# Kernel optimization log

Hardware: AMD Instinct MI355X
Metric: run time of the kernel (lower is better)

The kernel has to match this reference:

```python
import jax, jax.numpy as jnp
import numpy as np

EPS = 1e-16

def setup_inputs() -> dict:
    key = jax.random.key(0)
    k1, k2, k3, k4, k5, k6 = jax.random.split(key, 6)
    B, S, NT, E = 8, 256, 50, 64
    # sorted event times in [0, 90); horizon T = 100 > all events; all valid (>=0)
    event_times = jnp.sort(jax.random.uniform(k1, (B, S), dtype=jnp.float32) * 90.0, axis=1)
    event_types = jax.random.randint(k2, (B, S), 0, NT)
    # parameters initialized N(0, 0.1) as in _initialize_parameters
    type_embeddings = 0.1 * jax.random.normal(k3, (NT, E), dtype=jnp.float32)
    a = 0.1 * jax.random.normal(k4, (NT, E), dtype=jnp.float32)
    A = 0.1 * jax.random.normal(k5, (NT, NT, E), dtype=jnp.float32)
    P = 0.1 * jax.random.normal(k6, (NT, NT, E), dtype=jnp.float32)
    return {"event_times": event_times, "event_types": event_types, "T": 100,
            "type_embeddings": type_embeddings, "a": a, "A": A, "P": P}

def _hawkes_nll(event_times, event_types, T, emb, a, A, P):
    B, S = event_times.shape
    NT, E = emb.shape
    Tf = jnp.asarray(T, jnp.float32)
    emb_t = emb[event_types]            # (B,S,E) embedding of each event's type
    a_t = a[event_types]                # (B,S,E)
    valid = event_times >= 0.0          # (B,S)

    # ---- log-likelihood: intensity of the observed type at each event time ----
    # pairwise: axis 1 = query event i, axis 2 = history event j (j < i)
    dt = event_times[:, :, None] - event_times[:, None, :]                 # (B,Si,Sj)
    hist_mask = (jnp.arange(S)[:, None] > jnp.arange(S)[None, :])[None]    # (1,Si,Sj): j<i
    # A_pair[b,i,j,e] = A[type_j, type_i, e]; same for P_pair
    A_pair = A[event_types[:, None, :], event_types[:, :, None]]           # (B,Si,Sj,E)
    P_pair = P[event_types[:, None, :], event_types[:, :, None]]
    emb_i = emb_t[:, :, None, :]                                           # (B,Si,1,E)
    emb_j = emb_t[:, None, :, :]                                           # (B,1,Sj,E)
    decay = jnp.exp(-(emb_i * P_pair) * emb_j * dt[..., None])
    contrib = (emb_i * A_pair) * decay * emb_j                             # (B,Si,Sj,E)
    m = jnp.sum(jnp.where(hist_mask[..., None], contrib, 0.0), axis=2)     # (B,Si,E)
    inten = jnp.sum(jax.nn.softplus(emb_t * a_t + m), axis=-1)             # (B,S)
    ll = jnp.sum(jnp.where(valid, jnp.log(inten + EPS), 0.0))

    # ---- integral approximation (as in compute_loss) ----
    # intensity at horizon T for ALL types, using full valid history
    dT = Tf - event_times                                                  # (B,S)
    A_all = A[event_types]                                                 # (B,S,NT,E): A[t_j, t, e]
    P_all = P[event_types]
    decT = jnp.exp(-(emb[None, None] * P_all) * emb_t[:, :, None, :] * dT[:, :, None, None])
    conT = (emb[None, None] * A_all) * decT * emb_t[:, :, None, :]         # (B,S,NT,E)
    m_T = jnp.sum(jnp.where(valid[:, :, None, None], conT, 0.0), axis=1)   # (B,NT,E)
    inten_T = jnp.sum(jax.nn.softplus(emb * a + m_T), axis=(-2, -1))       # (B,)

    base_sum = jnp.sum(jax.nn.softplus(emb * a))                           # empty-history intensity summed over types
    any_valid = jnp.any(valid, axis=1)                                     # (B,)
    last_time = jnp.where(any_valid, jnp.max(jnp.where(valid, event_times, -1e30), axis=1), 0.0)
    first_time = jnp.where(any_valid, jnp.min(jnp.where(valid, event_times, 1e30), axis=1), 0.0)
    integ_b = jnp.where(any_valid,
                        inten_T * (Tf - last_time) + base_sum * first_time,
                        base_sum * Tf)
    integral = jnp.sum(integ_b)
    return -(ll - integral)

def reference(event_times, event_types, T, type_embeddings, a, A, P):
    return _hawkes_nll(event_times, event_types, T, type_embeddings, a, A, P)
```

## Files before the change

### kernel.cpp

```cpp
#include <hip/hip_runtime.h>
#include <math.h>

#define B   8
#define S   256
#define NT  50
#define E   64
#define NTE (NT * E)
#define EPSF 1e-16f

#define NW        4
#define LL_BLOCKS (B * S / 2)
#define IN_BLOCKS (B * NT)

__device__ __forceinline__ float softplus(float x) {
    if (x > 20.0f) return x;
    return log1pf(__expf(x));
}

__device__ __forceinline__ float wave_reduce_sum(float v) {
    #pragma unroll
    for (int off = 32; off > 0; off >>= 1)
        v += __shfl_down(v, off, 64);
    return v;
}

__global__ __launch_bounds__(64 * NW) void main_kernel(
    const float* __restrict__ times, const int* __restrict__ types,
    const int* __restrict__ Tp,
    const float* __restrict__ emb,  const float* __restrict__ a,
    const float* __restrict__ Amat, const float* __restrict__ Pmat,
    float* __restrict__ ws_ll, float* __restrict__ ws_int)
{
    const int tid = threadIdx.x;
    const int e   = tid & 63;
    const int w   = tid >> 6;
    const int bid = blockIdx.x;
    const bool is_ll = (bid < LL_BLOCKS);
    const int b = is_ll ? (bid / (S / 2)) : ((bid - LL_BLOCKS) / NT);

    __shared__ __align__(16) float s_emb[NTE];
    __shared__ float2 s_ev[S];
    __shared__ float  s_part[2][NW][E];
    __shared__ float  s_row[2];

    {
        const float4* __restrict__ emb4 = (const float4*)emb;
        float4* s4 = (float4*)s_emb;
        for (int idx = tid; idx < NTE / 4; idx += 64 * NW)
            s4[idx] = emb4[idx];
    }
    for (int j = tid; j < S; j += 64 * NW)
        s_ev[j] = make_float2(times[b * S + j], __int_as_float(types[b * S + j]));
    __syncthreads();

    if (is_ll) {
        const int ih = bid % (S / 2);
        const int rows[2] = { ih, S - 1 - ih };
        #pragma unroll
        for (int r = 0; r < 2; ++r) {
            const int   i     = rows[r];
            const float t_i   = s_ev[i].x;
            const int   ty_i  = __float_as_int(s_ev[i].y);
            const int   col   = ty_i * E + e;
            const float negEi = -s_emb[col];

            float macc = 0.0f;
            #pragma unroll 8
            for (int j = w; j < i; j += NW) {
                const float2 ev  = s_ev[j];
                const int   tyj  = __float_as_int(ev.y);
                const float dtj  = t_i - ev.x;
                const int   base = tyj * NTE + col;
                const float ej   = s_emb[tyj * E + e];
                const float Pe   = Pmat[base];
                const float Ae   = Amat[base];
                macc = fmaf(Ae * ej, __expf(negEi * Pe * ej * dtj), macc);
            }
            s_part[r][w][e] = macc;
        }
        __syncthreads();
        if (w < 2) {
            const int   i     = rows[w];
            const float t_i   = s_ev[i].x;
            const int   ty_i  = __float_as_int(s_ev[i].y);
            const int   col   = ty_i * E + e;
            const float emb_i = s_emb[col];
            float mt = 0.0f;
            #pragma unroll
            for (int q = 0; q < NW; ++q) mt += s_part[w][q][e];
            const float sp    = softplus(fmaf(emb_i, mt, emb_i * a[col]));
            const float inten = wave_reduce_sum(sp);
            if (e == 0)
                s_row[w] = (t_i >= 0.0f) ? logf(inten + EPSF) : 0.0f;
        }
        __syncthreads();
        if (tid == 0) ws_ll[bid] = s_row[0] + s_row[1];
    } else {
        const int   k    = (bid - LL_BLOCKS) % NT;
        const float Tf   = (float)(*Tp);
        const int   colk = k * E + e;
        const float embk = s_emb[colk];
        const float negEk = -embk;

        float acc = 0.0f;
        #pragma unroll 8
        for (int i = w; i < S; i += NW) {
            const float2 ev  = s_ev[i];
            const int   ty   = __float_as_int(ev.y);
            const float dT   = Tf - ev.x;
            const int   base = ty * NTE + colk;
            const float et   = s_emb[ty * E + e];
            const float c    = Amat[base] * et * __expf(negEk * Pmat[base] * et * dT);
            acc += (ev.x >= 0.0f) ? c : 0.0f;
        }
        s_part[0][w][e] = acc;
        __syncthreads();
        if (w == 0) {
            float mt = 0.0f;
            #pragma unroll
            for (int q = 0; q < NW; ++q) mt += s_part[0][q][e];
            const float sp = softplus(fmaf(embk, mt, embk * a[colk]));
            const float s  = wave_reduce_sum(sp);
            if (e == 0) ws_int[bid - LL_BLOCKS] = s;
        }
    }
}

__global__ __launch_bounds__(256) void finalize_kernel(
    const float* __restrict__ times,
    const int* __restrict__ Tp,
    const float* __restrict__ emb, const float* __restrict__ a,
    const float* __restrict__ ws_ll, const float* __restrict__ ws_int,
    float* __restrict__ out)
{
    const int t    = threadIdx.x;
    const int lane = t & 63;
    const int w    = t >> 6;
    const float Tf = (float)(*Tp);

    float llp = 0.0f;
    for (int idx = t; idx < LL_BLOCKS; idx += 256) llp += ws_ll[idx];
    float bs = 0.0f;
    for (int idx = t; idx < NTE; idx += 256) bs += softplus(emb[idx] * a[idx]);

    __shared__ float red[256], red2[256];
    red[t] = llp; red2[t] = bs;

    __shared__ float s_first[B], s_last[B], s_iT[B], s_any[B];
    for (int b = w; b < B; b += 4) {
        float mn = 1e30f, mx = -1e30f;
        #pragma unroll
        for (int q = 0; q < S / 64; ++q) {
            const float tv = times[b * S + q * 64 + lane];
            const bool valid = (tv >= 0.0f);
            mn = fminf(mn, valid ? tv : 1e30f);
            mx = fmaxf(mx, valid ? tv : -1e30f);
        }
        float iv = (lane < NT) ? ws_int[b * NT + lane] : 0.0f;
        #pragma unroll
        for (int off = 32; off > 0; off >>= 1) {
            mn = fminf(mn, __shfl_down(mn, off, 64));
            mx = fmaxf(mx, __shfl_down(mx, off, 64));
            iv += __shfl_down(iv, off, 64);
        }
        if (lane == 0) {
            const bool any_valid = (mn < 1e29f);
            s_any[b]   = any_valid ? 1.0f : 0.0f;
            s_first[b] = any_valid ? mn : 0.0f;
            s_last[b]  = any_valid ? mx : 0.0f;
            s_iT[b]    = iv;
        }
    }
    __syncthreads();

    for (int off = 128; off > 0; off >>= 1) {
        if (t < off) { red[t] += red[t + off]; red2[t] += red2[t + off]; }
        __syncthreads();
    }

    if (t == 0) {
        const float base_sum = red2[0];
        float integral = 0.0f;
        #pragma unroll
        for (int b = 0; b < B; ++b) {
            integral += (s_any[b] > 0.5f)
                ? s_iT[b] * (Tf - s_last[b]) + base_sum * s_first[b]
                : base_sum * Tf;
        }
        out[0] = integral - red[0];
    }
}

extern "C" void kernel_launch(void* const* d_in, const int* in_sizes, int n_in,
                              void* d_out, int out_size, void* d_ws, size_t ws_size,
                              hipStream_t stream) {
    const float* times = (const float*)d_in[0];
    const int*   types = (const int*)d_in[1];
    const int*   Tp    = (const int*)d_in[2];
    const float* emb   = (const float*)d_in[3];
    const float* a     = (const float*)d_in[4];
    const float* Amat  = (const float*)d_in[5];
    const float* Pmat  = (const float*)d_in[6];

    float* ws     = (float*)d_ws;
    float* ws_ll  = ws;
    float* ws_int = ws + LL_BLOCKS;
    float* out    = (float*)d_out;

    main_kernel<<<LL_BLOCKS + IN_BLOCKS, 64 * NW, 0, stream>>>(
        times, types, Tp, emb, a, Amat, Pmat, ws_ll, ws_int);
    finalize_kernel<<<1, 256, 0, stream>>>(times, Tp, emb, a, ws_ll, ws_int, out);
}
```

Baseline: 87.78 us.

## Fuse finalize into main kernel via last-block atomic and precompute type offsets

Removes the separate finalize kernel launch. Each block now increments a global counter, and the last block to finish runs the final reduction, then resets the counter. Event records in shared memory now hold precomputed type*E and type*NTE offsets so the inner loops skip the integer multiplies. The exponentials switch to exp2f with LOG2E folded into the per-row constant. The cost is one atomic and a threadfence per block, a wider shared-memory record, and reliance on the global counter being reset correctly between calls.

New measurement: 110.7 us. 26.1% more time.

```diff
diff --git a/kernel.cpp b/kernel.cpp
--- a/kernel.cpp
+++ b/kernel.cpp
@@ -7,10 +7,14 @@
 #define E   64
 #define NTE (NT * E)
 #define EPSF 1e-16f
+#define LOG2E 1.4426950408889634f
 
 #define NW        4
 #define LL_BLOCKS (B * S / 2)
 #define IN_BLOCKS (B * NT)
+#define NBLK      (LL_BLOCKS + IN_BLOCKS)
+
+__device__ int g_done = 0;
 
 __device__ __forceinline__ float softplus(float x) {
     if (x > 20.0f) return x;
@@ -29,7 +33,8 @@
     const int* __restrict__ Tp,
     const float* __restrict__ emb,  const float* __restrict__ a,
     const float* __restrict__ Amat, const float* __restrict__ Pmat,
-    float* __restrict__ ws_ll, float* __restrict__ ws_int)
+    float* __restrict__ ws_ll, float* __restrict__ ws_int,
+    float* __restrict__ out)
 {
     const int tid = threadIdx.x;
     const int e   = tid & 63;
@@ -38,10 +43,11 @@
     const bool is_ll = (bid < LL_BLOCKS);
     const int b = is_ll ? (bid / (S / 2)) : ((bid - LL_BLOCKS) / NT);
 
-    __shared__ __align__(16) float s_emb[NTE];
-    __shared__ float2 s_ev[S];
+    __shared__ __align__(16) float  s_emb[NTE];
+    __shared__ __align__(16) float4 s_ev[S];
     __shared__ float  s_part[2][NW][E];
     __shared__ float  s_row[2];
+    __shared__ int    s_fin;
 
     {
         const float4* __restrict__ emb4 = (const float4*)emb;
@@ -49,8 +55,12 @@
         for (int idx = tid; idx < NTE / 4; idx += 64 * NW)
             s4[idx] = emb4[idx];
     }
-    for (int j = tid; j < S; j += 64 * NW)
-        s_ev[j] = make_float2(times[b * S + j], __int_as_float(types[b * S + j]));
+    for (int j = tid; j < S; j += 64 * NW) {
+        const int ty = types[b * S + j];
+        s_ev[j] = make_float4(times[b * S + j],
+                              __int_as_float(ty * E),
+                              __int_as_float(ty * NTE), 0.0f);
+    }
     __syncthreads();
 
     if (is_ll) {
@@ -58,23 +68,21 @@
         const int rows[2] = { ih, S - 1 - ih };
         #pragma unroll
         for (int r = 0; r < 2; ++r) {
-            const int   i     = rows[r];
-            const float t_i   = s_ev[i].x;
-            const int   ty_i  = __float_as_int(s_ev[i].y);
-            const int   col   = ty_i * E + e;
-            const float negEi = -s_emb[col];
+            const int   i      = rows[r];
+            const float t_i    = s_ev[i].x;
+            const int   col    = __float_as_int(s_ev[i].y) + e;
+            const float negEi2 = -s_emb[col] * LOG2E;
 
             float macc = 0.0f;
             #pragma unroll 8
             for (int j = w; j < i; j += NW) {
-                const float2 ev  = s_ev[j];
-                const int   tyj  = __float_as_int(ev.y);
+                const float4 ev  = s_ev[j];
                 const float dtj  = t_i - ev.x;
-                const int   base = tyj * NTE + col;
-                const float ej   = s_emb[tyj * E + e];
+                const int   base = __float_as_int(ev.z) + col;
+                const float ej   = s_emb[__float_as_int(ev.y) + e];
                 const float Pe   = Pmat[base];
                 const float Ae   = Amat[base];
-                macc = fmaf(Ae * ej, __expf(negEi * Pe * ej * dtj), macc);
+                macc = fmaf(Ae * ej, exp2f(negEi2 * Pe * ej * dtj), macc);
             }
             s_part[r][w][e] = macc;
         }
@@ -82,8 +90,7 @@
         if (w < 2) {
             const int   i     = rows[w];
             const float t_i   = s_ev[i].x;
-            const int   ty_i  = __float_as_int(s_ev[i].y);
-            const int   col   = ty_i * E + e;
+            const int   col   = __float_as_int(s_ev[i].y) + e;
             const float emb_i = s_emb[col];
             float mt = 0.0f;
             #pragma unroll
@@ -96,21 +103,20 @@
         __syncthreads();
         if (tid == 0) ws_ll[bid] = s_row[0] + s_row[1];
     } else {
-        const int   k    = (bid - LL_BLOCKS) % NT;
-        const float Tf   = (float)(*Tp);
-        const int   colk = k * E + e;
-        const float embk = s_emb[colk];
-        const float negEk = -embk;
+        const int   k      = (bid - LL_BLOCKS) % NT;
+        const float Tf     = (float)(*Tp);
+        const int   colk   = k * E + e;
+        const float embk   = s_emb[colk];
+        const float negEk2 = -embk * LOG2E;
 
         float acc = 0.0f;
         #pragma unroll 8
         for (int i = w; i < S; i += NW) {
-            const float2 ev  = s_ev[i];
-            const int   ty   = __float_as_int(ev.y);
+            const float4 ev  = s_ev[i];
             const float dT   = Tf - ev.x;
-            const int   base = ty * NTE + colk;
-            const float et   = s_emb[ty * E + e];
-            const float c    = Amat[base] * et * __expf(negEk * Pmat[base] * et * dT);
+            const int   base = __float_as_int(ev.z) + colk;
+            const float et   = s_emb[__float_as_int(ev.y) + e];
+            const float c    = Amat[base] * et * exp2f(negEk2 * Pmat[base] * et * dT);
             acc += (ev.x >= 0.0f) ? c : 0.0f;
         }
         s_part[0][w][e] = acc;
@@ -124,39 +130,39 @@
             if (e == 0) ws_int[bid - LL_BLOCKS] = s;
         }
     }
-}
-
-__global__ __launch_bounds__(256) void finalize_kernel(
-    const float* __restrict__ times,
-    const int* __restrict__ Tp,
-    const float* __restrict__ emb, const float* __restrict__ a,
-    const float* __restrict__ ws_ll, const float* __restrict__ ws_int,
-    float* __restrict__ out)
-{
-    const int t    = threadIdx.x;
-    const int lane = t & 63;
-    const int w    = t >> 6;
+
+    if (tid == 0) {
+        __threadfence();
+        const int old = atomicAdd(&g_done, 1);
+        s_fin = (old == NBLK - 1) ? 1 : 0;
+    }
+    __syncthreads();
+    if (s_fin == 0) return;
+
+    __threadfence();
+
     const float Tf = (float)(*Tp);
 
     float llp = 0.0f;
-    for (int idx = t; idx < LL_BLOCKS; idx += 256) llp += ws_ll[idx];
+    for (int idx = tid; idx < LL_BLOCKS; idx += 256) llp += ws_ll[idx];
     float bs = 0.0f;
-    for (int idx = t; idx < NTE; idx += 256) bs += softplus(emb[idx] * a[idx]);
+    for (int idx = tid; idx < NTE; idx += 256) bs += softplus(s_emb[idx] * a[idx]);
 
     __shared__ float red[256], red2[256];
-    red[t] = llp; red2[t] = bs;
-
-    __shared__ float s_first[B], s_last[B], s_iT[B], s_any[B];
-    for (int b = w; b < B; b += 4) {
+    red[tid] = llp; red2[tid] = bs;
+
+    __shared__ float s_first[B], s_lastt[B], s_iT[B], s_any[B];
+    const int lane = tid & 63;
+    for (int bb = w; bb < B; bb += NW) {
         float mn = 1e30f, mx = -1e30f;
         #pragma unroll
         for (int q = 0; q < S / 64; ++q) {
-            const float tv = times[b * S + q * 64 + lane];
+            const float tv = times[bb * S + q * 64 + lane];
             const bool valid = (tv >= 0.0f);
             mn = fminf(mn, valid ? tv : 1e30f);
             mx = fmaxf(mx, valid ? tv : -1e30f);
         }
-        float iv = (lane < NT) ? ws_int[b * NT + lane] : 0.0f;
+        float iv = (lane < NT) ? ws_int[bb * NT + lane] : 0.0f;
         #pragma unroll
         for (int off = 32; off > 0; off >>= 1) {
             mn = fminf(mn, __shfl_down(mn, off, 64));
@@ -165,29 +171,30 @@
         }
         if (lane == 0) {
             const bool any_valid = (mn < 1e29f);
-            s_any[b]   = any_valid ? 1.0f : 0.0f;
-            s_first[b] = any_valid ? mn : 0.0f;
-            s_last[b]  = any_valid ? mx : 0.0f;
-            s_iT[b]    = iv;
+            s_any[bb]   = any_valid ? 1.0f : 0.0f;
+            s_first[bb] = any_valid ? mn : 0.0f;
+            s_lastt[bb] = any_valid ? mx : 0.0f;
+            s_iT[bb]    = iv;
         }
     }
     __syncthreads();
 
     for (int off = 128; off > 0; off >>= 1) {
-        if (t < off) { red[t] += red[t + off]; red2[t] += red2[t + off]; }
-        __syncthreads();
-    }
-
-    if (t == 0) {
+        if (tid < off) { red[tid] += red[tid + off]; red2[tid] += red2[tid + off]; }
+        __syncthreads();
+    }
+
+    if (tid == 0) {
         const float base_sum = red2[0];
         float integral = 0.0f;
         #pragma unroll
-        for (int b = 0; b < B; ++b) {
-            integral += (s_any[b] > 0.5f)
-                ? s_iT[b] * (Tf - s_last[b]) + base_sum * s_first[b]
+        for (int bb = 0; bb < B; ++bb) {
+            integral += (s_any[bb] > 0.5f)
+                ? s_iT[bb] * (Tf - s_lastt[bb]) + base_sum * s_first[bb]
                 : base_sum * Tf;
         }
         out[0] = integral - red[0];
+        atomicExch(&g_done, 0);
     }
 }
 
@@ -207,7 +214,6 @@
     float* ws_int = ws + LL_BLOCKS;
     float* out    = (float*)d_out;
 
-    main_kernel<<<LL_BLOCKS + IN_BLOCKS, 64 * NW, 0, stream>>>(
-        times, types, Tp, emb, a, Amat, Pmat, ws_ll, ws_int);
-    finalize_kernel<<<1, 256, 0, stream>>>(times, Tp, emb, a, ws_ll, ws_int, out);
-}
+    main_kernel<<<NBLK, 64 * NW, 0, stream>>>(
+        times, types, Tp, emb, a, Amat, Pmat, ws_ll, ws_int, out);
+}
```

## Stage per-row A/P slices in shared memory and use 8 waves per block

Applied to the files above, without the earlier changes.

Each block preloads the A and P columns for its query types (all source types) into LDS as interleaved float2. The inner loops then read from LDS instead of gathering from global memory. The block size doubles to 8 waves, and the exponential becomes exp2f with log2e folded into the scale. This adds large per-block staging traffic and about 51KB of LDS, which limits occupancy and may exceed the work the loop itself does.

Result: slower. 98.00 us (+11.6%).

```diff
diff --git a/kernel.cpp b/kernel.cpp
--- a/kernel.cpp
+++ b/kernel.cpp
@@ -7,8 +7,10 @@
 #define E   64
 #define NTE (NT * E)
 #define EPSF 1e-16f
-
-#define NW        4
+#define LOG2E 1.4426950408889634f
+
+#define NW        8
+#define NTHREADS  (64 * NW)
 #define LL_BLOCKS (B * S / 2)
 #define IN_BLOCKS (B * NT)
 
@@ -24,7 +26,7 @@
     return v;
 }
 
-__global__ __launch_bounds__(64 * NW) void main_kernel(
+__global__ __launch_bounds__(NTHREADS) void main_kernel(
     const float* __restrict__ times, const int* __restrict__ types,
     const int* __restrict__ Tp,
     const float* __restrict__ emb,  const float* __restrict__ a,
@@ -38,19 +40,40 @@
     const bool is_ll = (bid < LL_BLOCKS);
     const int b = is_ll ? (bid / (S / 2)) : ((bid - LL_BLOCKS) / NT);
 
-    __shared__ __align__(16) float s_emb[NTE];
+    __shared__ __align__(16) float  s_emb[NTE];
+    __shared__ __align__(16) float2 s_AP[2][NTE];
     __shared__ float2 s_ev[S];
     __shared__ float  s_part[2][NW][E];
     __shared__ float  s_row[2];
 
+    int ty0, ty1;
+    if (is_ll) {
+        const int ih = bid % (S / 2);
+        ty0 = types[b * S + ih];
+        ty1 = types[b * S + (S - 1 - ih)];
+    } else {
+        ty0 = (bid - LL_BLOCKS) % NT;
+        ty1 = ty0;
+    }
+
     {
         const float4* __restrict__ emb4 = (const float4*)emb;
         float4* s4 = (float4*)s_emb;
-        for (int idx = tid; idx < NTE / 4; idx += 64 * NW)
+        for (int idx = tid; idx < NTE / 4; idx += NTHREADS)
             s4[idx] = emb4[idx];
     }
-    for (int j = tid; j < S; j += 64 * NW)
-        s_ev[j] = make_float2(times[b * S + j], __int_as_float(types[b * S + j]));
+    for (int idx = tid; idx < NTE; idx += NTHREADS) {
+        const int row = idx >> 6, col = idx & 63;
+        const int g0 = row * NTE + ty0 * E + col;
+        s_AP[0][idx] = make_float2(Amat[g0], Pmat[g0]);
+        if (is_ll) {
+            const int g1 = row * NTE + ty1 * E + col;
+            s_AP[1][idx] = make_float2(Amat[g1], Pmat[g1]);
+        }
+    }
+    for (int j = tid; j < S; j += NTHREADS)
+        s_ev[j] = make_float2(times[b * S + j],
+                              __int_as_float(types[b * S + j] * E));
     __syncthreads();
 
     if (is_ll) {
@@ -58,23 +81,20 @@
         const int rows[2] = { ih, S - 1 - ih };
         #pragma unroll
         for (int r = 0; r < 2; ++r) {
-            const int   i     = rows[r];
-            const float t_i   = s_ev[i].x;
-            const int   ty_i  = __float_as_int(s_ev[i].y);
-            const int   col   = ty_i * E + e;
-            const float negEi = -s_emb[col];
+            const int   i      = rows[r];
+            const float t_i    = s_ev[i].x;
+            const int   col    = __float_as_int(s_ev[i].y) + e;
+            const float negEi2 = -s_emb[col] * LOG2E;
 
             float macc = 0.0f;
             #pragma unroll 8
             for (int j = w; j < i; j += NW) {
-                const float2 ev  = s_ev[j];
-                const int   tyj  = __float_as_int(ev.y);
-                const float dtj  = t_i - ev.x;
-                const int   base = tyj * NTE + col;
-                const float ej   = s_emb[tyj * E + e];
-                const float Pe   = Pmat[base];
-                const float Ae   = Amat[base];
-                macc = fmaf(Ae * ej, __expf(negEi * Pe * ej * dtj), macc);
+                const float2 ev   = s_ev[j];
+                const float  dtj  = t_i - ev.x;
+                const int    sidx = __float_as_int(ev.y) + e;
+                const float  ej   = s_emb[sidx];
+                const float2 ap   = s_AP[r][sidx];
+                macc = fmaf(ap.x * ej, exp2f(negEi2 * ap.y * ej * dtj), macc);
             }
             s_part[r][w][e] = macc;
         }
@@ -82,8 +102,7 @@
         if (w < 2) {
             const int   i     = rows[w];
             const float t_i   = s_ev[i].x;
-            const int   ty_i  = __float_as_int(s_ev[i].y);
-            const int   col   = ty_i * E + e;
+            const int   col   = __float_as_int(s_ev[i].y) + e;
             const float emb_i = s_emb[col];
             float mt = 0.0f;
             #pragma unroll
@@ -96,21 +115,20 @@
         __syncthreads();
         if (tid == 0) ws_ll[bid] = s_row[0] + s_row[1];
     } else {
-        const int   k    = (bid - LL_BLOCKS) % NT;
-        const float Tf   = (float)(*Tp);
-        const int   colk = k * E + e;
-        const float embk = s_emb[colk];
-        const float negEk = -embk;
+        const float Tf     = (float)(*Tp);
+        const int   colk   = ty0 * E + e;
+        const float embk   = s_emb[colk];
+        const float negEk2 = -embk * LOG2E;
 
         float acc = 0.0f;
         #pragma unroll 8
         for (int i = w; i < S; i += NW) {
-            const float2 ev  = s_ev[i];
-            const int   ty   = __float_as_int(ev.y);
-            const float dT   = Tf - ev.x;
-            const int   base = ty * NTE + colk;
-            const float et   = s_emb[ty * E + e];
-            const float c    = Amat[base] * et * __expf(negEk * Pmat[base] * et * dT);
+            const float2 ev   = s_ev[i];
+            const float  dT   = Tf - ev.x;
+            const int    sidx = __float_as_int(ev.y) + e;
+            const float  et   = s_emb[sidx];
+            const float2 ap   = s_AP[0][sidx];
+            const float  c    = ap.x * et * exp2f(negEk2 * ap.y * et * dT);
             acc += (ev.x >= 0.0f) ? c : 0.0f;
         }
         s_part[0][w][e] = acc;
@@ -207,7 +225,7 @@
     float* ws_int = ws + LL_BLOCKS;
     float* out    = (float*)d_out;
 
-    main_kernel<<<LL_BLOCKS + IN_BLOCKS, 64 * NW, 0, stream>>>(
+    main_kernel<<<LL_BLOCKS + IN_BLOCKS, NTHREADS, 0, stream>>>(
         times, types, Tp, emb, a, Amat, Pmat, ws_ll, ws_int);
     finalize_kernel<<<1, 256, 0, stream>>>(times, Tp, emb, a, ws_ll, ws_int, out);
 }
```

## Software-pipeline gathered A/P loads with double-buffered register groups

Applied to the files above, without the earlier changes.

The inner history loops are restructured into groups of 8 events whose A/P gathers are loaded into one register set while the previous group is computed, ping-ponging between two buffers. Per-event type offsets (ty*E, ty*NTE) are precomputed into a float4 shared-memory record, and the sums are split across two accumulators to shorten dependency chains. Launch bounds now request 3 blocks per SIMD. The aim is to hide global gather latency with more loads in flight, at the cost of higher register pressure and some masked wasted loads past the end of each row.

Result: slower. 120.9 us (+37.7%).

```diff
diff --git a/kernel.cpp b/kernel.cpp
--- a/kernel.cpp
+++ b/kernel.cpp
@@ -9,8 +9,10 @@
 #define EPSF 1e-16f
 
 #define NW        4
+#define NTHREADS  (64 * NW)
 #define LL_BLOCKS (B * S / 2)
 #define IN_BLOCKS (B * NT)
+#define G         8
 
 __device__ __forceinline__ float softplus(float x) {
     if (x > 20.0f) return x;
@@ -24,7 +26,40 @@
     return v;
 }
 
-__global__ __launch_bounds__(64 * NW) void main_kernel(
+#define LOADG(g, TT, EE, AA, PP) do {                                       \
+    _Pragma("unroll")                                                       \
+    for (int q = 0; q < G; ++q) {                                           \
+        const int s  = (g) * G + q;                                         \
+        const int jj = (w + s * NW) & (S - 1);                              \
+        const float4 ev = s_ev[jj];             \
+        TT[q] = ev.x;                                                       \
+        EE[q] = s_emb[__float_as_int(ev.y) + e];                            \
+        const int  idx = __float_as_int(ev.z) + col;                        \
+        const bool ok  = (s < scnt);                \
+        AA[q] = ok ? Amat[idx] : 0.0f;                                      \
+        PP[q] = ok ? Pmat[idx] : 0.0f;                                      \
+    } } while (0)
+
+#define COMPG_LL(TT, EE, AA, PP) do {                                       \
+    _Pragma("unroll")                                                       \
+    for (int q = 0; q < G; ++q) {                                           \
+        const float dt = t_i - TT[q];                                       \
+        const float ex = __expf(negEi * PP[q] * EE[q] * dt);                \
+        if (q & 1) m1 = fmaf(AA[q] * EE[q], ex, m1);                        \
+        else       m0 = fmaf(AA[q] * EE[q], ex, m0);                        \
+    } } while (0)
+
+#define COMPG_IN(TT, EE, AA, PP) do {                                       \
+    _Pragma("unroll")                                                       \
+    for (int q = 0; q < G; ++q) {                                           \
+        const float dT = Tf - TT[q];                                        \
+        const float ex = __expf(negEk * PP[q] * EE[q] * dT);                \
+        const float c  = AA[q] * EE[q] * ex;                                \
+        if (q & 1) a1 += (TT[q] >= 0.0f) ? c : 0.0f;                        \
+        else       a0 += (TT[q] >= 0.0f) ? c : 0.0f;                        \
+    } } while (0)
+
+__global__ __launch_bounds__(NTHREADS, 3) void main_kernel(
     const float* __restrict__ times, const int* __restrict__ types,
     const int* __restrict__ Tp,
     const float* __restrict__ emb,  const float* __restrict__ a,
@@ -38,19 +73,23 @@
     const bool is_ll = (bid < LL_BLOCKS);
     const int b = is_ll ? (bid / (S / 2)) : ((bid - LL_BLOCKS) / NT);
 
-    __shared__ __align__(16) float s_emb[NTE];
-    __shared__ float2 s_ev[S];
-    __shared__ float  s_part[2][NW][E];
-    __shared__ float  s_row[2];
+    __shared__ __align__(16) float  s_emb[NTE];
+    __shared__ __align__(16) float4 s_ev[S];
+    __shared__ float s_part[2][NW][E];
+    __shared__ float s_row[2];
 
     {
         const float4* __restrict__ emb4 = (const float4*)emb;
         float4* s4 = (float4*)s_emb;
-        for (int idx = tid; idx < NTE / 4; idx += 64 * NW)
+        for (int idx = tid; idx < NTE / 4; idx += NTHREADS)
             s4[idx] = emb4[idx];
     }
-    for (int j = tid; j < S; j += 64 * NW)
-        s_ev[j] = make_float2(times[b * S + j], __int_as_float(types[b * S + j]));
+    for (int j = tid; j < S; j += NTHREADS) {
+        const int ty = types[b * S + j];
+        s_ev[j] = make_float4(times[b * S + j],
+                              __int_as_float(ty * E),
+                              __int_as_float(ty * NTE), 0.0f);
+    }
     __syncthreads();
 
     if (is_ll) {
@@ -60,30 +99,28 @@
         for (int r = 0; r < 2; ++r) {
             const int   i     = rows[r];
             const float t_i   = s_ev[i].x;
-            const int   ty_i  = __float_as_int(s_ev[i].y);
-            const int   col   = ty_i * E + e;
+            const int   col   = __float_as_int(s_ev[i].y) + e;
             const float negEi = -s_emb[col];
-
-            float macc = 0.0f;
-            #pragma unroll 8
-            for (int j = w; j < i; j += NW) {
-                const float2 ev  = s_ev[j];
-                const int   tyj  = __float_as_int(ev.y);
-                const float dtj  = t_i - ev.x;
-                const int   base = tyj * NTE + col;
-                const float ej   = s_emb[tyj * E + e];
-                const float Pe   = Pmat[base];
-                const float Ae   = Amat[base];
-                macc = fmaf(Ae * ej, __expf(negEi * Pe * ej * dtj), macc);
+            const int scnt = (i > w) ? ((i - w + NW - 1) / NW) : 0;
+            const int ngp  = (scnt + G - 1) / G;
+
+            float m0 = 0.0f, m1 = 0.0f;
+            float TA[G], EA[G], Aa[G], PA[G];
+            float TB[G], EB[G], Ab[G], PB[G];
+            LOADG(0, TA, EA, Aa, PA);
+            for (int g = 0; g < ngp; g += 2) {
+                LOADG(g + 1, TB, EB, Ab, PB);
+                COMPG_LL(TA, EA, Aa, PA);
+                LOADG(g + 2, TA, EA, Aa, PA);
+                COMPG_LL(TB, EB, Ab, PB);
             }
-            s_part[r][w][e] = macc;
+            s_part[r][w][e] = m0 + m1;
         }
         __syncthreads();
         if (w < 2) {
             const int   i     = rows[w];
             const float t_i   = s_ev[i].x;
-            const int   ty_i  = __float_as_int(s_ev[i].y);
-            const int   col   = ty_i * E + e;
+            const int   col   = __float_as_int(s_ev[i].y) + e;
             const float emb_i = s_emb[col];
             float mt = 0.0f;
             #pragma unroll
@@ -96,32 +133,33 @@
         __syncthreads();
         if (tid == 0) ws_ll[bid] = s_row[0] + s_row[1];
     } else {
-        const int   k    = (bid - LL_BLOCKS) % NT;
-        const float Tf   = (float)(*Tp);
-        const int   colk = k * E + e;
-        const float embk = s_emb[colk];
+        const int   k     = (bid - LL_BLOCKS) % NT;
+        const float Tf    = (float)(*Tp);
+        const int   col   = k * E + e;
+        const float embk  = s_emb[col];
         const float negEk = -embk;
-
-        float acc = 0.0f;
-        #pragma unroll 8
-        for (int i = w; i < S; i += NW) {
-            const float2 ev  = s_ev[i];
-            const int   ty   = __float_as_int(ev.y);
-            const float dT   = Tf - ev.x;
-            const int   base = ty * NTE + colk;
-            const float et   = s_emb[ty * E + e];
-            const float c    = Amat[base] * et * __expf(negEk * Pmat[base] * et * dT);
-            acc += (ev.x >= 0.0f) ? c : 0.0f;
-        }
-        s_part[0][w][e] = acc;
+        const int scnt = (S - w + NW - 1) / NW;
+        const int ngp  = (scnt + G - 1) / G;
+
+        float a0 = 0.0f, a1 = 0.0f;
+        float TA[G], EA[G], Aa[G], PA[G];
+        float TB[G], EB[G], Ab[G], PB[G];
+        LOADG(0, TA, EA, Aa, PA);
+        for (int g = 0; g < ngp; g += 2) {
+            LOADG(g + 1, TB, EB, Ab, PB);
+            COMPG_IN(TA, EA, Aa, PA);
+            LOADG(g + 2, TA, EA, Aa, PA);
+            COMPG_IN(TB, EB, Ab, PB);
+        }
+        s_part[0][w][e] = a0 + a1;
         __syncthreads();
         if (w == 0) {
             float mt = 0.0f;
             #pragma unroll
             for (int q = 0; q < NW; ++q) mt += s_part[0][q][e];
-            const float sp = softplus(fmaf(embk, mt, embk * a[colk]));
-            const float s  = wave_reduce_sum(sp);
-            if (e == 0) ws_int[bid - LL_BLOCKS] = s;
+            const float sp = softplus(fmaf(embk, mt, embk * a[col]));
+            const float ss = wave_reduce_sum(sp);
+            if (e == 0) ws_int[bid - LL_BLOCKS] = ss;
         }
     }
 }
@@ -207,7 +245,7 @@
     float* ws_int = ws + LL_BLOCKS;
     float* out    = (float*)d_out;
 
-    main_kernel<<<LL_BLOCKS + IN_BLOCKS, 64 * NW, 0, stream>>>(
+    main_kernel<<<LL_BLOCKS + IN_BLOCKS, NTHREADS, 0, stream>>>(
         times, types, Tp, emb, a, Amat, Pmat, ws_ll, ws_int);
     finalize_kernel<<<1, 256, 0, stream>>>(times, Tp, emb, a, ws_ll, ws_int, out);
 }
```
